# Optimization experiments

Hardware: AMD Instinct MI355X
Metric: run time of the kernel (lower is better)

## Reference

```python
import jax, jax.numpy as jnp
import numpy as np

EPS = 1e-5

def _lc(x, w, b, stride, pad):
    # x: [B,H,W]; w: [Ho,Wo,kh,kw]; b: [Ho,Wo]
    Ho, Wo, kh, kw = w.shape
    patches = jax.lax.conv_general_dilated_patches(
        x[:, None], (kh, kw), (stride, stride), [(pad, pad), (pad, pad)])
    # patches: [B, kh*kw, Ho, Wo]
    out = jnp.einsum('bkij,ijk->bij', patches, w.reshape(Ho, Wo, kh * kw))
    return out + b

def _ln2d(x, g, b):
    # torch LayerNorm over the last two (spatial) dims
    mu = x.mean(axis=(1, 2), keepdims=True)
    var = ((x - mu) ** 2).mean(axis=(1, 2), keepdims=True)
    return (x - mu) * jax.lax.rsqrt(var + EPS) * g + b

def _pool(x):
    # MaxPool2d(kernel=2, stride=2) over spatial dims of [B,H,W]
    return jax.lax.reduce_window(x, -jnp.inf, jax.lax.max, (1, 2, 2), (1, 2, 2), 'VALID')

def setup_inputs() -> dict:
    key = jax.random.key(0)
    ks = jax.random.split(key, 32)
    d = {}
    d['x'] = jax.random.normal(ks[0], (64, 128, 128), jnp.float32)
    sizes = [(128, 7), (64, 5), (64, 5), (32, 3), (32, 3), (16, 3)]
    for i, (s, k) in enumerate(sizes, start=1):
        d[f'w{i}'] = jax.random.normal(ks[4 * i], (s, s, k, k), jnp.float32) / k
        d[f'b{i}'] = jax.random.normal(ks[4 * i + 1], (s, s), jnp.float32)
        d[f'g{i}'] = jnp.ones((s, s), jnp.float32)
        d[f'be{i}'] = jnp.zeros((s, s), jnp.float32)
    d['fcw'] = jax.random.normal(ks[30], (1024, 256), jnp.float32) / np.sqrt(256.0)
    d['fcb'] = jax.random.normal(ks[31], (1024,), jnp.float32) * 0.01
    return d

def reference(x, w1, b1, g1, be1, w2, b2, g2, be2, w3, b3, g3, be3,
              w4, b4, g4, be4, w5, b5, g5, be5, w6, b6, g6, be6, fcw, fcb):
    # dropout is identity (eval / p=0)
    h = _pool(_ln2d(jax.nn.relu(_lc(x, w1, b1, 1, 3)), g1, be1))   # [B,64,64]
    h = _ln2d(jax.nn.relu(_lc(h, w2, b2, 1, 2)), g2, be2)          # [B,64,64]
    h = _pool(_ln2d(jax.nn.relu(_lc(h, w3, b3, 1, 2)), g3, be3))   # [B,32,32]
    h = _ln2d(jax.nn.relu(_lc(h, w4, b4, 1, 1)), g4, be4)          # [B,32,32]
    h = _pool(_ln2d(jax.nn.relu(_lc(h, w5, b5, 1, 1)), g5, be5))   # [B,16,16]
    h = _ln2d(jax.nn.relu(_lc(h, w6, b6, 1, 1)), g6, be6)          # [B,16,16]
    h = h.reshape(h.shape[0], -1) @ fcw.T + fcb                    # [B,1024]
    return jax.nn.softmax(h, axis=-1)
```

## Files before the change

### kernel.cpp

```cpp
#include <hip/hip_runtime.h>

#define LN_EPS 1e-5f

constexpr int T1_OFF   = 0;
constexpr int WT2_OFF  = 1048576;
constexpr int WT3_OFF  = WT2_OFF + 102400;
constexpr int WT4_OFF  = WT3_OFF + 102400;
constexpr int WT5_OFF  = WT4_OFF + 9216;
constexpr int WT6_OFF  = WT5_OFF + 9216;
constexpr int FCWT_OFF = WT6_OFF + 2304;

constexpr int NREP = 136;

__global__ __launch_bounds__(256) void s1_conv(const float* __restrict__ x,
                                               const float* __restrict__ w1,
                                               const float* __restrict__ b1,
                                               const float* __restrict__ w2,
                                               const float* __restrict__ w3,
                                               const float* __restrict__ w4,
                                               const float* __restrict__ w5,
                                               const float* __restrict__ w6,
                                               const float* __restrict__ fcw,
                                               float* __restrict__ ws)
{
    const int tid = threadIdx.x;

    if (blockIdx.x < NREP) {
        const int rb = blockIdx.x;
        if (rb < 32) {
            for (int idx = rb * 256 + tid; idx < 102400; idx += 32 * 256) {
                int p = idx / 25, k = idx % 25;
                ws[WT2_OFF + k * 4096 + p] = w2[idx];
            }
        } else if (rb < 64) {
            for (int idx = (rb - 32) * 256 + tid; idx < 102400; idx += 32 * 256) {
                int p = idx / 25, k = idx % 25;
                ws[WT3_OFF + k * 4096 + p] = w3[idx];
            }
        } else if (rb < 68) {
            for (int idx = (rb - 64) * 256 + tid; idx < 9216; idx += 4 * 256) {
                int p = idx / 9, k = idx % 9;
                ws[WT4_OFF + k * 1024 + p] = w4[idx];
            }
        } else if (rb < 72) {
            for (int idx = (rb - 68) * 256 + tid; idx < 9216; idx += 4 * 256) {
                int p = idx / 9, k = idx % 9;
                ws[WT5_OFF + k * 1024 + p] = w5[idx];
            }
        } else if (rb < 73) {
            for (int idx = tid; idx < 2304; idx += 256) {
                int p = idx / 9, k = idx % 9;
                ws[WT6_OFF + k * 256 + p] = w6[idx];
            }
        } else {
            for (int idx = (rb - 73) * 256 + tid; idx < 262144; idx += 63 * 256) {
                int r = idx >> 8, kc = idx & 255;
                int kq = kc >> 2, c = kc & 3;
                ws[FCWT_OFF + kq * 4096 + r * 4 + c] = fcw[idx];
            }
        }
        return;
    }

    constexpr int R = 128, K = 7, TILE = 8, S = 16, PAD = 3;
    constexpr int RT = TILE + K - 1;
    constexpr int PP = RT * RT + 1;
    constexpr int NBLK = R / TILE;
    constexpr int WCNT = TILE * TILE * K * K;
    constexpr int PG = 256 / S;
    constexpr int OPT = TILE * TILE / PG;

    __shared__ float s_in[S * PP];
    __shared__ float s_w[WCNT];
    __shared__ float s_b[TILE * TILE];

    float* t1 = ws + T1_OFF;
    const int cb = blockIdx.x - NREP;
    const int bt = cb % (NBLK * NBLK);
    const int sg = cb / (NBLK * NBLK);
    const int i0 = (bt / NBLK) * TILE;
    const int j0 = (bt % NBLK) * TILE;
    const int S0 = sg * S;

    for (int idx = tid; idx < WCNT; idx += 256) {
        int pi = idx / (K * K), kk = idx % (K * K);
        int gi = i0 + pi / TILE, gj = j0 + pi % TILE;
        s_w[idx] = w1[(gi * R + gj) * (K * K) + kk];
    }
    if (tid < TILE * TILE)
        s_b[tid] = b1[(i0 + tid / TILE) * R + (j0 + tid % TILE)];

    for (int idx = tid; idx < S * RT * RT; idx += 256) {
        int ls = idx / (RT * RT), p = idx % (RT * RT);
        int ci = i0 - PAD + p / RT, cj = j0 - PAD + p % RT;
        float v = 0.0f;
        if (ci >= 0 && ci < R && cj >= 0 && cj < R)
            v = x[(S0 + ls) * R * R + ci * R + cj];
        s_in[ls * PP + p] = v;
    }
    __syncthreads();

    const int s = tid % S;
    const int pg = tid / S;
    const int p0 = pg * OPT;
    const int ti = p0 / TILE, tj0 = p0 % TILE;
    float acc[OPT];
    #pragma unroll
    for (int o = 0; o < OPT; o++) acc[o] = s_b[p0 + o];
    #pragma unroll
    for (int ki = 0; ki < K; ki++) {
        float row[OPT + K - 1];
        #pragma unroll
        for (int c = 0; c < OPT + K - 1; c++)
            row[c] = s_in[s * PP + (ti + ki) * RT + tj0 + c];
        #pragma unroll
        for (int kj = 0; kj < K; kj++)
            #pragma unroll
            for (int o = 0; o < OPT; o++)
                acc[o] += row[o + kj] * s_w[(p0 + o) * (K * K) + ki * K + kj];
    }
    #pragma unroll
    for (int o = 0; o < OPT; o++)
        t1[(S0 + s) * R * R + (i0 + ti) * R + (j0 + tj0 + o)] = fmaxf(acc[o], 0.0f);
}

constexpr int NT = 1024;
constexpr int NW = NT / 64;

__device__ __forceinline__ void stats_reduce(float* red, float lsum, float lsq,
                                             float inv_n, float* s_mu, float* s_rs)
{
    const int tid = threadIdx.x;
    #pragma unroll
    for (int off = 32; off > 0; off >>= 1) {
        lsum += __shfl_down(lsum, off, 64);
        lsq  += __shfl_down(lsq,  off, 64);
    }
    if ((tid & 63) == 0) { red[tid >> 6] = lsum; red[NW + (tid >> 6)] = lsq; }
    __syncthreads();
    if (tid == 0) {
        float a = 0.f, b = 0.f;
        #pragma unroll
        for (int i = 0; i < NW; i++) { a += red[i]; b += red[NW + i]; }
        float mu = a * inv_n, ms = b * inv_n;
        *s_mu = mu;
        *s_rs = rsqrtf(ms - mu * mu + LN_EPS);
    }
    __syncthreads();
}

template<int M, int K>
__device__ __forceinline__ void conv_lds(const float* __restrict__ I,
                                         const float* __restrict__ wT,
                                         const float* __restrict__ bias,
                                         float* __restrict__ R,
                                         float& lsum, float& lsq)
{
    constexpr int NPOS = M * M;
    constexpr int PADK = (K - 1) / 2;
    constexpr int STR = M + 1;
    constexpr int OPT = (NPOS + NT - 1) / NT;
    const int tid = threadIdx.x;

    #pragma unroll
    for (int o = 0; o < OPT; o++) {
        int p = tid + o * NT;
        if (NPOS < NT && p >= NPOS) break;
        int i = p / M, j = p % M;
        float acc = bias[p];
        #pragma unroll
        for (int ki = 0; ki < K; ki++) {
            int ii = i - PADK + ki;
            bool rok = (ii >= 0 && ii < M);
            #pragma unroll
            for (int kj = 0; kj < K; kj++) {
                int jj = j - PADK + kj;
                float iv = (rok && jj >= 0 && jj < M) ? I[ii * STR + jj] : 0.0f;
                acc += iv * wT[(ki * K + kj) * NPOS + p];
            }
        }
        float v = fmaxf(acc, 0.0f);
        R[i * STR + j] = v;
        lsum += v;
        lsq  += v * v;
    }
}

template<int N, bool POOL>
__device__ __forceinline__ void transform(const float* __restrict__ R,
                                          float mu, float rs,
                                          const float* __restrict__ g,
                                          const float* __restrict__ b,
                                          float* __restrict__ I)
{
    constexpr int M = POOL ? N / 2 : N;
    constexpr int SR = N + 1, SI = M + 1;
    const int tid = threadIdx.x;
    for (int p = tid; p < M * M; p += NT) {
        int i = p / M, j = p % M;
        float v;
        if constexpr (POOL) {
            float best = -3.4e38f;
            #pragma unroll
            for (int dy = 0; dy < 2; dy++)
                #pragma unroll
                for (int dx = 0; dx < 2; dx++) {
                    int r = 2 * i + dy, c = 2 * j + dx;
                    float n = (R[r * SR + c] - mu) * rs * g[r * N + c] + b[r * N + c];
                    best = fmaxf(best, n);
                }
            v = best;
        } else {
            v = (R[i * SR + j] - mu) * rs * g[i * N + j] + b[i * N + j];
        }
        I[i * SI + j] = v;
    }
}

__global__ __launch_bounds__(1024) void tail_fused(
    const float* __restrict__ ws_ro,
    const float* __restrict__ g1, const float* __restrict__ be1,
    const float* __restrict__ b2,
    const float* __restrict__ g2, const float* __restrict__ be2,
    const float* __restrict__ b3,
    const float* __restrict__ g3, const float* __restrict__ be3,
    const float* __restrict__ b4,
    const float* __restrict__ g4, const float* __restrict__ be4,
    const float* __restrict__ b5,
    const float* __restrict__ g5, const float* __restrict__ be5,
    const float* __restrict__ b6,
    const float* __restrict__ g6, const float* __restrict__ be6,
    const float* __restrict__ fcb,
    float* __restrict__ outp)
{
    __shared__ __align__(16) float I[64 * 65];
    __shared__ __align__(16) float R[64 * 65];
    __shared__ __align__(16) float h[256];
    __shared__ float red[2 * NW];
    __shared__ float s_mu, s_rs;

    const int s = blockIdx.x;
    const int tid = threadIdx.x;
    const float* x1  = ws_ro + T1_OFF + s * 16384;
    const float* wT2 = ws_ro + WT2_OFF;
    const float* wT3 = ws_ro + WT3_OFF;
    const float* wT4 = ws_ro + WT4_OFF;
    const float* wT5 = ws_ro + WT5_OFF;
    const float* wT6 = ws_ro + WT6_OFF;

    float ls = 0.f, lq = 0.f;
    {
        const float4* x4 = (const float4*)x1;
        #pragma unroll
        for (int i = tid; i < 4096; i += NT) {
            float4 v = x4[i];
            ls += v.x + v.y + v.z + v.w;
            lq += v.x * v.x + v.y * v.y + v.z * v.z + v.w * v.w;
        }
    }
    stats_reduce(red, ls, lq, 1.f / 16384.f, &s_mu, &s_rs);

    {
        float mu = s_mu, rs = s_rs;
        #pragma unroll
        for (int o = 0; o < 4; o++) {
            int p = tid + o * NT;
            int i = p >> 6, j = p & 63;
            float2 xa = *((const float2*)(x1 + (2 * i) * 128 + 2 * j));
            float2 xb = *((const float2*)(x1 + (2 * i + 1) * 128 + 2 * j));
            float2 ga = *((const float2*)(g1 + (2 * i) * 128 + 2 * j));
            float2 gb = *((const float2*)(g1 + (2 * i + 1) * 128 + 2 * j));
            float2 ba = *((const float2*)(be1 + (2 * i) * 128 + 2 * j));
            float2 bb = *((const float2*)(be1 + (2 * i + 1) * 128 + 2 * j));
            float n0 = (xa.x - mu) * rs * ga.x + ba.x;
            float n1 = (xa.y - mu) * rs * ga.y + ba.y;
            float n2 = (xb.x - mu) * rs * gb.x + bb.x;
            float n3 = (xb.y - mu) * rs * gb.y + bb.y;
            I[i * 65 + j] = fmaxf(fmaxf(n0, n1), fmaxf(n2, n3));
        }
    }
    __syncthreads();

    float ls2, lq2;

    ls2 = lq2 = 0.f; conv_lds<64, 5>(I, wT2, b2, R, ls2, lq2);
    stats_reduce(red, ls2, lq2, 1.f / 4096.f, &s_mu, &s_rs);
    transform<64, false>(R, s_mu, s_rs, g2, be2, I);
    __syncthreads();

    ls2 = lq2 = 0.f; conv_lds<64, 5>(I, wT3, b3, R, ls2, lq2);
    stats_reduce(red, ls2, lq2, 1.f / 4096.f, &s_mu, &s_rs);
    transform<64, true>(R, s_mu, s_rs, g3, be3, I);
    __syncthreads();

    ls2 = lq2 = 0.f; conv_lds<32, 3>(I, wT4, b4, R, ls2, lq2);
    stats_reduce(red, ls2, lq2, 1.f / 1024.f, &s_mu, &s_rs);
    transform<32, false>(R, s_mu, s_rs, g4, be4, I);
    __syncthreads();

    ls2 = lq2 = 0.f; conv_lds<32, 3>(I, wT5, b5, R, ls2, lq2);
    stats_reduce(red, ls2, lq2, 1.f / 1024.f, &s_mu, &s_rs);
    transform<32, true>(R, s_mu, s_rs, g5, be5, I);
    __syncthreads();

    ls2 = lq2 = 0.f; conv_lds<16, 3>(I, wT6, b6, R, ls2, lq2);
    stats_reduce(red, ls2, lq2, 1.f / 256.f, &s_mu, &s_rs);

    if (tid < 256) {
        int i = tid >> 4, j = tid & 15;
        h[tid] = (R[i * 17 + j] - s_mu) * s_rs * g6[tid] + be6[tid];
    }
    __syncthreads();

    float acc = fcb[tid];
    {
        const float4* wq = (const float4*)(ws_ro + FCWT_OFF);
        const float4* h4 = (const float4*)h;
        #pragma unroll 8
        for (int kq = 0; kq < 64; kq++) {
            float4 wv = wq[kq * 1024 + tid];
            float4 hv = h4[kq];
            acc += wv.x * hv.x + wv.y * hv.y + wv.z * hv.z + wv.w * hv.w;
        }
    }

    float m = acc;
    #pragma unroll
    for (int off = 32; off > 0; off >>= 1)
        m = fmaxf(m, __shfl_down(m, off, 64));
    if ((tid & 63) == 0) red[tid >> 6] = m;
    __syncthreads();
    if (tid == 0) {
        float mm = red[0];
        #pragma unroll
        for (int i = 1; i < NW; i++) mm = fmaxf(mm, red[i]);
        s_mu = mm;
    }
    __syncthreads();
    float e = expf(acc - s_mu);
    float sum = e;
    #pragma unroll
    for (int off = 32; off > 0; off >>= 1)
        sum += __shfl_down(sum, off, 64);
    if ((tid & 63) == 0) red[NW + (tid >> 6)] = sum;
    __syncthreads();
    if (tid == 0) {
        float ss = 0.f;
        #pragma unroll
        for (int i = 0; i < NW; i++) ss += red[NW + i];
        s_rs = 1.0f / ss;
    }
    __syncthreads();
    outp[s * 1024 + tid] = e * s_rs;
}

extern "C" void kernel_launch(void* const* d_in, const int* in_sizes, int n_in,
                              void* d_out, int out_size, void* d_ws, size_t ws_size,
                              hipStream_t stream) {
    (void)in_sizes; (void)n_in; (void)out_size; (void)ws_size;

    const float* x   = (const float*)d_in[0];
    const float* w1  = (const float*)d_in[1];  const float* b1  = (const float*)d_in[2];
    const float* g1  = (const float*)d_in[3];  const float* be1 = (const float*)d_in[4];
    const float* w2  = (const float*)d_in[5];  const float* b2  = (const float*)d_in[6];
    const float* g2  = (const float*)d_in[7];  const float* be2 = (const float*)d_in[8];
    const float* w3  = (const float*)d_in[9];  const float* b3  = (const float*)d_in[10];
    const float* g3  = (const float*)d_in[11]; const float* be3 = (const float*)d_in[12];
    const float* w4  = (const float*)d_in[13]; const float* b4  = (const float*)d_in[14];
    const float* g4  = (const float*)d_in[15]; const float* be4 = (const float*)d_in[16];
    const float* w5  = (const float*)d_in[17]; const float* b5  = (const float*)d_in[18];
    const float* g5  = (const float*)d_in[19]; const float* be5 = (const float*)d_in[20];
    const float* w6  = (const float*)d_in[21]; const float* b6  = (const float*)d_in[22];
    const float* g6  = (const float*)d_in[23]; const float* be6 = (const float*)d_in[24];
    const float* fcw = (const float*)d_in[25]; const float* fcb = (const float*)d_in[26];

    float* ws = (float*)d_ws;

    s1_conv<<<NREP + 1024, 256, 0, stream>>>(x, w1, b1, w2, w3, w4, w5, w6, fcw, ws);
    tail_fused<<<64, 1024, 0, stream>>>((const float*)ws,
        g1, be1, b2, g2, be2, b3, g3, be3,
        b4, g4, be4, b5, g5, be5, b6, g6, be6,
        fcb, (float*)d_out);
}
```

Baseline: 155.6 us.

## Split fused per-sample tail into per-stage multi-block conv kernels

Replaces the single 64-block tail kernel (one 1024-thread block per sample running layers 2-6) with separate per-layer kernels that split each sample into 8-row slabs, giving 256-512 blocks per stage. LayerNorm statistics are produced as per-block partial sums written to the workspace, and the next stage reduces them before applying normalize and pool while loading its halo slab. The first conv kernel also emits these partial stats. This aims to fill the GPU's compute units that sat idle with only 64 blocks, at the cost of extra kernel launches and global-memory round trips for intermediates.

```diff
diff --git a/kernel.cpp b/kernel.cpp
--- a/kernel.cpp
+++ b/kernel.cpp
@@ -9,6 +9,15 @@
 constexpr int WT5_OFF  = WT4_OFF + 9216;
 constexpr int WT6_OFF  = WT5_OFF + 9216;
 constexpr int FCWT_OFF = WT6_OFF + 2304;
+constexpr int R2_OFF   = FCWT_OFF + 262144;
+constexpr int R3_OFF   = R2_OFF + 262144;
+constexpr int R4_OFF   = R3_OFF + 262144;
+constexpr int R5_OFF   = R4_OFF + 65536;
+constexpr int ST1_OFF  = R5_OFF + 65536;
+constexpr int ST2_OFF  = ST1_OFF + 32768;
+constexpr int ST3_OFF  = ST2_OFF + 1024;
+constexpr int ST4_OFF  = ST3_OFF + 1024;
+constexpr int ST5_OFF  = ST4_OFF + 512;
 
 constexpr int NREP = 136;
 
@@ -73,6 +82,7 @@
     __shared__ float s_in[S * PP];
     __shared__ float s_w[WCNT];
     __shared__ float s_b[TILE * TILE];
+    __shared__ float sp[4][16], sq[4][16];
 
     float* t1 = ws + T1_OFF;
     const int cb = blockIdx.x - NREP;
@@ -119,9 +129,130 @@
             for (int o = 0; o < OPT; o++)
                 acc[o] += row[o + kj] * s_w[(p0 + o) * (K * K) + ki * K + kj];
     }
-    #pragma unroll
-    for (int o = 0; o < OPT; o++)
-        t1[(S0 + s) * R * R + (i0 + ti) * R + (j0 + tj0 + o)] = fmaxf(acc[o], 0.0f);
+    float lsum = 0.f, lsq = 0.f;
+    #pragma unroll
+    for (int o = 0; o < OPT; o++) {
+        float v = fmaxf(acc[o], 0.0f);
+        t1[(S0 + s) * R * R + (i0 + ti) * R + (j0 + tj0 + o)] = v;
+        lsum += v; lsq += v * v;
+    }
+    lsum += __shfl_xor(lsum, 16, 64); lsum += __shfl_xor(lsum, 32, 64);
+    lsq  += __shfl_xor(lsq,  16, 64); lsq  += __shfl_xor(lsq,  32, 64);
+    const int w = tid >> 6, l = tid & 63;
+    if (l < 16) { sp[w][l] = lsum; sq[w][l] = lsq; }
+    __syncthreads();
+    if (tid < 16) {
+        float a = sp[0][tid] + sp[1][tid] + sp[2][tid] + sp[3][tid];
+        float b = sq[0][tid] + sq[1][tid] + sq[2][tid] + sq[3][tid];
+        ws[ST1_OFF + (S0 + tid) * 512 + bt * 2]     = a;
+        ws[ST1_OFF + (S0 + tid) * 512 + bt * 2 + 1] = b;
+    }
+}
+
+__device__ __forceinline__ void block_sum2_256(float a, float b, float* red)
+{
+    const int tid = threadIdx.x;
+    #pragma unroll
+    for (int off = 32; off > 0; off >>= 1) {
+        a += __shfl_down(a, off, 64);
+        b += __shfl_down(b, off, 64);
+    }
+    if ((tid & 63) == 0) { red[tid >> 6] = a; red[4 + (tid >> 6)] = b; }
+    __syncthreads();
+    if (tid == 0) {
+        red[0] = red[0] + red[1] + red[2] + red[3];
+        red[4] = red[4] + red[5] + red[6] + red[7];
+    }
+    __syncthreads();
+}
+
+template<int M, int K, bool POOL>
+__global__ __launch_bounds__(256) void stage_conv(
+    const float* __restrict__ wsr, float* __restrict__ wsw,
+    const float* __restrict__ g, const float* __restrict__ be,
+    const float* __restrict__ bias,
+    int inOff, int wtOff, int outOff,
+    int stInOff, int nStatIn, float invNIn, int stOutOff)
+{
+    constexpr int NSLAB  = M / 8;
+    constexpr int PADK   = (K - 1) / 2;
+    constexpr int HR     = 8 + 2 * PADK;
+    constexpr int IN_RES = POOL ? 2 * M : M;
+    constexpr int STR    = M + 1;
+
+    __shared__ float Isl[HR * STR];
+    __shared__ float red[8];
+
+    const int tid  = threadIdx.x;
+    const int s    = blockIdx.x / NSLAB;
+    const int slab = blockIdx.x % NSLAB;
+    const int r0   = slab * 8;
+
+    float a = 0.f, b = 0.f;
+    for (int t = tid; t < nStatIn; t += 256) {
+        a += wsr[stInOff + (s * nStatIn + t) * 2];
+        b += wsr[stInOff + (s * nStatIn + t) * 2 + 1];
+    }
+    block_sum2_256(a, b, red);
+    const float mu = red[0] * invNIn;
+    const float rs = rsqrtf(red[4] * invNIn - mu * mu + LN_EPS);
+
+    const float* In = wsr + inOff + s * (IN_RES * IN_RES);
+
+    for (int idx = tid; idx < HR * M; idx += 256) {
+        int lr = idx / M, jc = idx % M;
+        int gr = r0 - PADK + lr;
+        float v = 0.f;
+        if (gr >= 0 && gr < M) {
+            if constexpr (POOL) {
+                float2 xa = *(const float2*)(In + (2 * gr) * IN_RES + 2 * jc);
+                float2 xb = *(const float2*)(In + (2 * gr + 1) * IN_RES + 2 * jc);
+                float2 ga = *(const float2*)(g  + (2 * gr) * IN_RES + 2 * jc);
+                float2 gb = *(const float2*)(g  + (2 * gr + 1) * IN_RES + 2 * jc);
+                float2 ea = *(const float2*)(be + (2 * gr) * IN_RES + 2 * jc);
+                float2 eb = *(const float2*)(be + (2 * gr + 1) * IN_RES + 2 * jc);
+                float n0 = (xa.x - mu) * rs * ga.x + ea.x;
+                float n1 = (xa.y - mu) * rs * ga.y + ea.y;
+                float n2 = (xb.x - mu) * rs * gb.x + eb.x;
+                float n3 = (xb.y - mu) * rs * gb.y + eb.y;
+                v = fmaxf(fmaxf(n0, n1), fmaxf(n2, n3));
+            } else {
+                int q = gr * M + jc;
+                v = (In[q] - mu) * rs * g[q] + be[q];
+            }
+        }
+        Isl[lr * STR + jc] = v;
+    }
+    __syncthreads();
+
+    const float* wT = wsr + wtOff;
+    constexpr int OPW = (8 * M) / 256;
+    float lsum = 0.f, lsq = 0.f;
+    #pragma unroll
+    for (int o = 0; o < OPW; o++) {
+        int p  = tid + o * 256;
+        int li = p / M, j = p % M;
+        int gi = r0 + li;
+        int gp = gi * M + j;
+        float acc = bias[gp];
+        #pragma unroll
+        for (int ki = 0; ki < K; ki++)
+            #pragma unroll
+            for (int kj = 0; kj < K; kj++) {
+                int jj = j - PADK + kj;
+                float iv = (jj >= 0 && jj < M) ? Isl[(li + ki) * STR + jj] : 0.f;
+                acc += iv * wT[(ki * K + kj) * (M * M) + gp];
+            }
+        float v = fmaxf(acc, 0.f);
+        wsw[outOff + s * (M * M) + gp] = v;
+        lsum += v; lsq += v * v;
+    }
+    __syncthreads();
+    block_sum2_256(lsum, lsq, red);
+    if (tid == 0) {
+        wsw[stOutOff + (s * NSLAB + slab) * 2]     = red[0];
+        wsw[stOutOff + (s * NSLAB + slab) * 2 + 1] = red[4];
+    }
 }
 
 constexpr int NT = 1024;
@@ -149,172 +280,79 @@
     __syncthreads();
 }
 
-template<int M, int K>
-__device__ __forceinline__ void conv_lds(const float* __restrict__ I,
-                                         const float* __restrict__ wT,
-                                         const float* __restrict__ bias,
-                                         float* __restrict__ R,
-                                         float& lsum, float& lsq)
-{
-    constexpr int NPOS = M * M;
-    constexpr int PADK = (K - 1) / 2;
-    constexpr int STR = M + 1;
-    constexpr int OPT = (NPOS + NT - 1) / NT;
-    const int tid = threadIdx.x;
-
-    #pragma unroll
-    for (int o = 0; o < OPT; o++) {
-        int p = tid + o * NT;
-        if (NPOS < NT && p >= NPOS) break;
-        int i = p / M, j = p % M;
-        float acc = bias[p];
-        #pragma unroll
-        for (int ki = 0; ki < K; ki++) {
-            int ii = i - PADK + ki;
-            bool rok = (ii >= 0 && ii < M);
-            #pragma unroll
-            for (int kj = 0; kj < K; kj++) {
-                int jj = j - PADK + kj;
-                float iv = (rok && jj >= 0 && jj < M) ? I[ii * STR + jj] : 0.0f;
-                acc += iv * wT[(ki * K + kj) * NPOS + p];
-            }
-        }
-        float v = fmaxf(acc, 0.0f);
-        R[i * STR + j] = v;
-        lsum += v;
-        lsq  += v * v;
-    }
-}
-
-template<int N, bool POOL>
-__device__ __forceinline__ void transform(const float* __restrict__ R,
-                                          float mu, float rs,
-                                          const float* __restrict__ g,
-                                          const float* __restrict__ b,
-                                          float* __restrict__ I)
-{
-    constexpr int M = POOL ? N / 2 : N;
-    constexpr int SR = N + 1, SI = M + 1;
-    const int tid = threadIdx.x;
-    for (int p = tid; p < M * M; p += NT) {
-        int i = p / M, j = p % M;
-        float v;
-        if constexpr (POOL) {
-            float best = -3.4e38f;
-            #pragma unroll
-            for (int dy = 0; dy < 2; dy++)
-                #pragma unroll
-                for (int dx = 0; dx < 2; dx++) {
-                    int r = 2 * i + dy, c = 2 * j + dx;
-                    float n = (R[r * SR + c] - mu) * rs * g[r * N + c] + b[r * N + c];
-                    best = fmaxf(best, n);
-                }
-            v = best;
-        } else {
-            v = (R[i * SR + j] - mu) * rs * g[i * N + j] + b[i * N + j];
-        }
-        I[i * SI + j] = v;
-    }
-}
-
-__global__ __launch_bounds__(1024) void tail_fused(
-    const float* __restrict__ ws_ro,
-    const float* __restrict__ g1, const float* __restrict__ be1,
-    const float* __restrict__ b2,
-    const float* __restrict__ g2, const float* __restrict__ be2,
-    const float* __restrict__ b3,
-    const float* __restrict__ g3, const float* __restrict__ be3,
-    const float* __restrict__ b4,
-    const float* __restrict__ g4, const float* __restrict__ be4,
-    const float* __restrict__ b5,
+__global__ __launch_bounds__(1024) void s6_tail(
+    const float* __restrict__ wsr,
     const float* __restrict__ g5, const float* __restrict__ be5,
     const float* __restrict__ b6,
     const float* __restrict__ g6, const float* __restrict__ be6,
     const float* __restrict__ fcb,
     float* __restrict__ outp)
 {
-    __shared__ __align__(16) float I[64 * 65];
-    __shared__ __align__(16) float R[64 * 65];
-    __shared__ __align__(16) float h[256];
+    __shared__ float I6[16 * 17];
+    __shared__ float h[256];
     __shared__ float red[2 * NW];
     __shared__ float s_mu, s_rs;
 
     const int s = blockIdx.x;
     const int tid = threadIdx.x;
-    const float* x1  = ws_ro + T1_OFF + s * 16384;
-    const float* wT2 = ws_ro + WT2_OFF;
-    const float* wT3 = ws_ro + WT3_OFF;
-    const float* wT4 = ws_ro + WT4_OFF;
-    const float* wT5 = ws_ro + WT5_OFF;
-    const float* wT6 = ws_ro + WT6_OFF;
-
-    float ls = 0.f, lq = 0.f;
-    {
-        const float4* x4 = (const float4*)x1;
-        #pragma unroll
-        for (int i = tid; i < 4096; i += NT) {
-            float4 v = x4[i];
-            ls += v.x + v.y + v.z + v.w;
-            lq += v.x * v.x + v.y * v.y + v.z * v.z + v.w * v.w;
+
+    if (tid == 0) {
+        float a = 0.f, b = 0.f;
+        #pragma unroll
+        for (int i = 0; i < 4; i++) {
+            a += wsr[ST5_OFF + (s * 4 + i) * 2];
+            b += wsr[ST5_OFF + (s * 4 + i) * 2 + 1];
         }
-    }
-    stats_reduce(red, ls, lq, 1.f / 16384.f, &s_mu, &s_rs);
-
-    {
-        float mu = s_mu, rs = s_rs;
-        #pragma unroll
-        for (int o = 0; o < 4; o++) {
-            int p = tid + o * NT;
-            int i = p >> 6, j = p & 63;
-            float2 xa = *((const float2*)(x1 + (2 * i) * 128 + 2 * j));
-            float2 xb = *((const float2*)(x1 + (2 * i + 1) * 128 + 2 * j));
-            float2 ga = *((const float2*)(g1 + (2 * i) * 128 + 2 * j));
-            float2 gb = *((const float2*)(g1 + (2 * i + 1) * 128 + 2 * j));
-            float2 ba = *((const float2*)(be1 + (2 * i) * 128 + 2 * j));
-            float2 bb = *((const float2*)(be1 + (2 * i + 1) * 128 + 2 * j));
-            float n0 = (xa.x - mu) * rs * ga.x + ba.x;
-            float n1 = (xa.y - mu) * rs * ga.y + ba.y;
-            float n2 = (xb.x - mu) * rs * gb.x + bb.x;
-            float n3 = (xb.y - mu) * rs * gb.y + bb.y;
-            I[i * 65 + j] = fmaxf(fmaxf(n0, n1), fmaxf(n2, n3));
-        }
-    }
-    __syncthreads();
-
-    float ls2, lq2;
-
-    ls2 = lq2 = 0.f; conv_lds<64, 5>(I, wT2, b2, R, ls2, lq2);
-    stats_reduce(red, ls2, lq2, 1.f / 4096.f, &s_mu, &s_rs);
-    transform<64, false>(R, s_mu, s_rs, g2, be2, I);
-    __syncthreads();
-
-    ls2 = lq2 = 0.f; conv_lds<64, 5>(I, wT3, b3, R, ls2, lq2);
-    stats_reduce(red, ls2, lq2, 1.f / 4096.f, &s_mu, &s_rs);
-    transform<64, true>(R, s_mu, s_rs, g3, be3, I);
-    __syncthreads();
-
-    ls2 = lq2 = 0.f; conv_lds<32, 3>(I, wT4, b4, R, ls2, lq2);
-    stats_reduce(red, ls2, lq2, 1.f / 1024.f, &s_mu, &s_rs);
-    transform<32, false>(R, s_mu, s_rs, g4, be4, I);
-    __syncthreads();
-
-    ls2 = lq2 = 0.f; conv_lds<32, 3>(I, wT5, b5, R, ls2, lq2);
-    stats_reduce(red, ls2, lq2, 1.f / 1024.f, &s_mu, &s_rs);
-    transform<32, true>(R, s_mu, s_rs, g5, be5, I);
-    __syncthreads();
-
-    ls2 = lq2 = 0.f; conv_lds<16, 3>(I, wT6, b6, R, ls2, lq2);
-    stats_reduce(red, ls2, lq2, 1.f / 256.f, &s_mu, &s_rs);
+        float mu = a * (1.f / 1024.f);
+        s_mu = mu;
+        s_rs = rsqrtf(b * (1.f / 1024.f) - mu * mu + LN_EPS);
+    }
+    __syncthreads();
+    const float mu5 = s_mu, rs5 = s_rs;
+    const float* R5 = wsr + R5_OFF + s * 1024;
 
     if (tid < 256) {
         int i = tid >> 4, j = tid & 15;
-        h[tid] = (R[i * 17 + j] - s_mu) * s_rs * g6[tid] + be6[tid];
-    }
+        float2 xa = *(const float2*)(R5 + (2 * i) * 32 + 2 * j);
+        float2 xb = *(const float2*)(R5 + (2 * i + 1) * 32 + 2 * j);
+        float2 ga = *(const float2*)(g5 + (2 * i) * 32 + 2 * j);
+        float2 gb = *(const float2*)(g5 + (2 * i + 1) * 32 + 2 * j);
+        float2 ea = *(const float2*)(be5 + (2 * i) * 32 + 2 * j);
+        float2 eb = *(const float2*)(be5 + (2 * i + 1) * 32 + 2 * j);
+        float n0 = (xa.x - mu5) * rs5 * ga.x + ea.x;
+        float n1 = (xa.y - mu5) * rs5 * ga.y + ea.y;
+        float n2 = (xb.x - mu5) * rs5 * gb.x + eb.x;
+        float n3 = (xb.y - mu5) * rs5 * gb.y + eb.y;
+        I6[i * 17 + j] = fmaxf(fmaxf(n0, n1), fmaxf(n2, n3));
+    }
+    __syncthreads();
+
+    float v = 0.f, ls = 0.f, lq = 0.f;
+    if (tid < 256) {
+        int i = tid >> 4, j = tid & 15;
+        const float* wT6 = wsr + WT6_OFF;
+        float acc = b6[tid];
+        #pragma unroll
+        for (int ki = 0; ki < 3; ki++) {
+            int ii = i - 1 + ki;
+            bool rok = (ii >= 0 && ii < 16);
+            #pragma unroll
+            for (int kj = 0; kj < 3; kj++) {
+                int jj = j - 1 + kj;
+                float iv = (rok && jj >= 0 && jj < 16) ? I6[ii * 17 + jj] : 0.f;
+                acc += iv * wT6[(ki * 3 + kj) * 256 + tid];
+            }
+        }
+        v = fmaxf(acc, 0.f);
+        ls = v; lq = v * v;
+    }
+    stats_reduce(red, ls, lq, 1.f / 256.f, &s_mu, &s_rs);
+    if (tid < 256) h[tid] = (v - s_mu) * s_rs * g6[tid] + be6[tid];
     __syncthreads();
 
     float acc = fcb[tid];
     {
-        const float4* wq = (const float4*)(ws_ro + FCWT_OFF);
+        const float4* wq = (const float4*)(wsr + FCWT_OFF);
         const float4* h4 = (const float4*)h;
         #pragma unroll 8
         for (int kq = 0; kq < 64; kq++) {
@@ -377,8 +415,16 @@
     float* ws = (float*)d_ws;
 
     s1_conv<<<NREP + 1024, 256, 0, stream>>>(x, w1, b1, w2, w3, w4, w5, w6, fcw, ws);
-    tail_fused<<<64, 1024, 0, stream>>>((const float*)ws,
-        g1, be1, b2, g2, be2, b3, g3, be3,
-        b4, g4, be4, b5, g5, be5, b6, g6, be6,
-        fcb, (float*)d_out);
-}
+
+    stage_conv<64, 5, true ><<<512, 256, 0, stream>>>(ws, ws, g1, be1, b2,
+        T1_OFF, WT2_OFF, R2_OFF, ST1_OFF, 256, 1.f / 16384.f, ST2_OFF);
+    stage_conv<64, 5, false><<<512, 256, 0, stream>>>(ws, ws, g2, be2, b3,
+        R2_OFF, WT3_OFF, R3_OFF, ST2_OFF, 8, 1.f / 4096.f, ST3_OFF);
+    stage_conv<32, 3, true ><<<256, 256, 0, stream>>>(ws, ws, g3, be3, b4,
+        R3_OFF, WT4_OFF, R4_OFF, ST3_OFF, 8, 1.f / 4096.f, ST4_OFF);
+    stage_conv<32, 3, false><<<256, 256, 0, stream>>>(ws, ws, g4, be4, b5,
+        R4_OFF, WT5_OFF, R5_OFF, ST4_OFF, 4, 1.f / 1024.f, ST5_OFF);
+
+    s6_tail<<<64, 1024, 0, stream>>>((const float*)ws,
+        g5, be5, b6, g6, be6, fcb, (float*)d_out);
+}
```

Result: no change. 156.8 us (+0.8%).
